# Performance work log

Hardware: AMD Instinct MI355X
Metric: run time of the kernel (lower is better)

The kernel has to match this reference:

```python
import jax, jax.numpy as jnp
import numpy as np

NEG = 1e12


def _sincos(seq_len, dim):
    # SinusoidalPositionEmbedding with merge_mode='zero': [1, S, dim] interleaved (sin, cos)
    pos = jnp.arange(seq_len, dtype=jnp.float32)
    inv = jnp.power(10000.0, -2.0 * jnp.arange(dim // 2, dtype=jnp.float32) / dim)
    emb = pos[:, None] * inv[None, :]                      # [S, dim/2]
    emb = jnp.stack([jnp.sin(emb), jnp.cos(emb)], axis=-1).reshape(seq_len, dim)
    cos_pos = jnp.repeat(emb[:, 1::2], 2, axis=-1)[None]   # [1, S, dim]
    sin_pos = jnp.repeat(emb[:, ::2], 2, axis=-1)[None]    # [1, S, dim]
    return cos_pos, sin_pos


def _rope(x, cos_pos, sin_pos):
    # x: [B, S, d]; rotate pairs: (-x1, x0, -x3, x2, ...)
    x2 = jnp.stack([-x[..., 1::2], x[..., ::2]], axis=-1).reshape(x.shape)
    return x * cos_pos + x2 * sin_pos


def _pointer_head(hidden, mask_f, W1, b1, W2, b2, inner_dim):
    B, S, _ = hidden.shape
    out = hidden @ W1 + b1                                 # [B, S, 2*inner_dim]
    qw, kw = out[..., ::2], out[..., 1::2]                 # [B, S, inner_dim]
    cos_pos, sin_pos = _sincos(S, inner_dim)
    qw = _rope(qw, cos_pos, sin_pos)
    kw = _rope(kw, cos_pos, sin_pos)
    logits = jnp.einsum('bmd,bnd->bmn', qw, kw) / (inner_dim ** 0.5)  # [B, S, S]
    bias = jnp.transpose(hidden @ W2 + b2, (0, 2, 1)) / 2.0           # [B, 2T, S]
    # [B, T, S, S]
    logits = logits[:, None] + bias[:, ::2, None, :] + bias[:, 1::2, :, None]
    # sequence masking on key axis (last) and query axis (second-to-last)
    mk = mask_f[:, None, None, :]
    mq = mask_f[:, None, :, None]
    logits = logits * mq - NEG * (1.0 - mq)
    logits = logits * mk - NEG * (1.0 - mk)
    # strict lower-triangular mask over (m, n)
    tril = jnp.tril(jnp.ones((S, S), dtype=logits.dtype), k=-1)
    logits = logits - tril * NEG
    return logits


def setup_inputs() -> dict:
    key = jax.random.key(0)
    ks = jax.random.split(key, 10)
    B, S, H = 8, 512, 768
    inner_dim, ent_t, arg_t = 64, 12, 16
    s = 0.02
    return {
        'last_hidden_state': jax.random.normal(ks[0], (B, S, H), jnp.float32),
        'attention_mask': jnp.ones((B, S), jnp.int32),
        'W1': jax.random.normal(ks[1], (H, inner_dim * 2), jnp.float32) * s,
        'b1': jax.random.normal(ks[2], (inner_dim * 2,), jnp.float32) * s,
        'W2': jax.random.normal(ks[3], (H, ent_t * 2), jnp.float32) * s,
        'b2': jax.random.normal(ks[4], (ent_t * 2,), jnp.float32) * s,
        'Wa1': jax.random.normal(ks[5], (H, inner_dim * 2), jnp.float32) * s,
        'ba1': jax.random.normal(ks[6], (inner_dim * 2,), jnp.float32) * s,
        'Wa2': jax.random.normal(ks[7], (H, arg_t * 2), jnp.float32) * s,
        'ba2': jax.random.normal(ks[8], (arg_t * 2,), jnp.float32) * s,
    }


def reference(last_hidden_state, attention_mask, W1, b1, W2, b2, Wa1, ba1, Wa2, ba2):
    inner_dim = W1.shape[1] // 2
    mask_f = attention_mask.astype(last_hidden_state.dtype)
    logits = _pointer_head(last_hidden_state, mask_f, W1, b1, W2, b2, inner_dim)
    argument_logits = _pointer_head(last_hidden_state, mask_f, Wa1, ba1, Wa2, ba2, inner_dim)
    return logits, argument_logits
```

## Files before the change

### kernel.cpp

```cpp
#include <hip/hip_runtime.h>
#include <hip/hip_bf16.h>

typedef __attribute__((ext_vector_type(8))) short s16x8;
typedef __attribute__((ext_vector_type(4))) float f32x4;

#define NEGC 1000000000000.0f

constexpr int B_ = 8, S_ = 512, H_ = 768;
constexpr int ENT = 12, ARG = 16;
constexpr int NC = 320;
constexpr int ROWS = B_ * S_;
constexpr size_t OUT_ENT = (size_t)B_ * ENT * S_ * S_;

static __device__ __forceinline__ unsigned short f2bf(float x) {
  return __builtin_bit_cast(unsigned short, __float2bfloat16(x));
}

__global__ __launch_bounds__(256) void k_prep(
    const float* __restrict__ X,
    const float* __restrict__ W1, const float* __restrict__ b1,
    const float* __restrict__ W2, const float* __restrict__ b2,
    const float* __restrict__ Wa1, const float* __restrict__ ba1,
    const float* __restrict__ Wa2, const float* __restrict__ ba2,
    __hip_bfloat16* __restrict__ Xb,
    __hip_bfloat16* __restrict__ Wt,
    float* __restrict__ bcat) {
  int idx = blockIdx.x * 256 + threadIdx.x;
  const int nx = ROWS * H_ / 4;
  if (idx < nx) {
    float4 v = reinterpret_cast<const float4*>(X)[idx];
    ushort4 o;
    o.x = f2bf(v.x); o.y = f2bf(v.y); o.z = f2bf(v.z); o.w = f2bf(v.w);
    reinterpret_cast<ushort4*>(Xb)[idx] = o;
    return;
  }
  idx -= nx;
  if (idx < NC * H_) {
    int n = idx / H_;
    int k = idx - n * H_;
    float v = 0.0f;
    if (n < 128)      v = W1[k * 128 + n];
    else if (n < 152) v = W2[k * 24 + (n - 128)];
    else if (n < 280) v = Wa1[k * 128 + (n - 152)];
    else if (n < 312) v = Wa2[k * 32 + (n - 280)];
    reinterpret_cast<unsigned short*>(Wt)[(size_t)n * H_ + k] = f2bf(v);
    return;
  }
  idx -= NC * H_;
  if (idx < NC) {
    int n = idx;
    float v = 0.0f;
    if (n < 128)      v = b1[n];
    else if (n < 152) v = b2[n - 128];
    else if (n < 280) v = ba1[n - 152];
    else if (n < 312) v = ba2[n - 280];
    bcat[n] = v;
  }
}

__global__ __launch_bounds__(256) void k_gemm(
    const __hip_bfloat16* __restrict__ Xb,
    const __hip_bfloat16* __restrict__ Wt,
    const float* __restrict__ bcat,
    __hip_bfloat16* __restrict__ qwe, __hip_bfloat16* __restrict__ kwe,
    __hip_bfloat16* __restrict__ qwa, __hip_bfloat16* __restrict__ kwa,
    float* __restrict__ kbe, float* __restrict__ qbe,
    float* __restrict__ kba, float* __restrict__ qba) {
  const int lane = threadIdx.x & 63;
  const int wid  = threadIdx.x >> 6;
  const int row0 = blockIdx.y * 64 + (wid >> 1) * 32;
  const int col0 = blockIdx.x * 64 + (wid & 1) * 32;
  const int rl   = lane & 15;
  const int rg   = lane >> 4;
  const int kseg = rg * 8;
  const short* Ws = reinterpret_cast<const short*>(Wt);
  const short* Xs = reinterpret_cast<const short*>(Xb);
  f32x4 acc[2][2] = {};
#pragma unroll 4
  for (int kk = 0; kk < H_; kk += 32) {
    s16x8 a[2], bb[2];
#pragma unroll
    for (int ni = 0; ni < 2; ++ni)
      a[ni] = *reinterpret_cast<const s16x8*>(Ws + (size_t)(col0 + ni * 16 + rl) * H_ + kk + kseg);
#pragma unroll
    for (int mj = 0; mj < 2; ++mj)
      bb[mj] = *reinterpret_cast<const s16x8*>(Xs + (size_t)(row0 + mj * 16 + rl) * H_ + kk + kseg);
#pragma unroll
    for (int ni = 0; ni < 2; ++ni)
#pragma unroll
      for (int mj = 0; mj < 2; ++mj)
        acc[ni][mj] = __builtin_amdgcn_mfma_f32_16x16x32_bf16(a[ni], bb[mj], acc[ni][mj], 0, 0, 0);
  }
#pragma unroll
  for (int ni = 0; ni < 2; ++ni) {
    const int nq = col0 + ni * 16 + rg * 4;
    if (nq >= 312) continue;
    float4 bc = *reinterpret_cast<const float4*>(bcat + nq);
#pragma unroll
    for (int mj = 0; mj < 2; ++mj) {
      const int r = row0 + mj * 16 + rl;
      const int b = r >> 9, mm = r & 511;
      float v0 = acc[ni][mj][0] + bc.x;
      float v1 = acc[ni][mj][1] + bc.y;
      float v2 = acc[ni][mj][2] + bc.z;
      float v3 = acc[ni][mj][3] + bc.w;
      if (nq < 128 || (nq >= 152 && nq < 280)) {
        const bool ent = nq < 128;
        const int p = (ent ? nq : nq - 152) >> 2;
        float inv = exp2f(-(float)p * 0.4152410118609203f);
        float s, c;
        sincosf((float)mm * inv, &s, &c);
        unsigned int qpk = (unsigned int)f2bf(v0 * c - v2 * s) |
                           ((unsigned int)f2bf(v2 * c + v0 * s) << 16);
        unsigned int kpk = (unsigned int)f2bf(v1 * c - v3 * s) |
                           ((unsigned int)f2bf(v3 * c + v1 * s) << 16);
        short* qd = reinterpret_cast<short*>(ent ? qwe : qwa);
        short* kd = reinterpret_cast<short*>(ent ? kwe : kwa);
        *reinterpret_cast<unsigned int*>(qd + (size_t)r * 64 + 2 * p) = qpk;
        *reinterpret_cast<unsigned int*>(kd + (size_t)r * 64 + 2 * p) = kpk;
      } else {
        const bool ent = nq < 152;
        const int base = ent ? 128 : 280;
        const int T = ent ? ENT : ARG;
        float* qb = ent ? qbe : qba;
        float* kb = ent ? kbe : kba;
        float vv[4] = {v0, v1, v2, v3};
#pragma unroll
        for (int q = 0; q < 4; ++q) {
          int e = nq - base + q;
          int t = e >> 1;
          float* dst = (e & 1) ? qb : kb;
          dst[((size_t)b * T + t) * S_ + mm] = vv[q] * 0.5f;
        }
      }
    }
  }
}

__global__ __launch_bounds__(256) void k_bcast(
    const __hip_bfloat16* __restrict__ qwe, const __hip_bfloat16* __restrict__ kwe,
    const __hip_bfloat16* __restrict__ qwa, const __hip_bfloat16* __restrict__ kwa,
    const float* __restrict__ kbe, const float* __restrict__ qbe,
    const float* __restrict__ kba, const float* __restrict__ qba,
    const int* __restrict__ mask,
    float* __restrict__ out) {
  const int lane = threadIdx.x & 63;
  const int w = threadIdx.x >> 6;
  const int b = blockIdx.z;
  const int m0 = blockIdx.y * 64 + w * 16;
  const int n0 = blockIdx.x * 64;
  const int col = lane & 15;
  const int rg = lane >> 4;
  const int kseg = rg * 8;

  int mrow[4];
  float mqv[4], sqv[4];
#pragma unroll
  for (int j = 0; j < 4; ++j) {
    mrow[j] = m0 + rg * 4 + j;
    float mf = (float)mask[b * S_ + mrow[j]];
    mqv[j] = mf; sqv[j] = NEGC * (1.0f - mf);
  }
  int ncol[4];
  float mkv[4], skv[4];
#pragma unroll
  for (int f = 0; f < 4; ++f) {
    ncol[f] = n0 + 16 * f + col;
    float mf = (float)mask[b * S_ + ncol[f]];
    mkv[f] = mf; skv[f] = NEGC * (1.0f - mf);
  }
  float M[4][4], O[4][4];
#pragma unroll
  for (int f = 0; f < 4; ++f)
#pragma unroll
    for (int j = 0; j < 4; ++j) {
      M[f][j] = mqv[j] * mkv[f];
      O[f][j] = sqv[j] * mkv[f] + skv[f] + ((ncol[f] < mrow[j]) ? NEGC : 0.0f);
    }

  auto head = [&](const __hip_bfloat16* qw, const __hip_bfloat16* kw,
                  const float* qb, const float* kb, int T, size_t obase0) {
    const short* qs = reinterpret_cast<const short*>(qw);
    const short* ks = reinterpret_cast<const short*>(kw);
    f32x4 acc[4] = {};
#pragma unroll
    for (int kk = 0; kk < 64; kk += 32) {
      s16x8 a = *reinterpret_cast<const s16x8*>(
          qs + (size_t)(b * S_ + m0 + col) * 64 + kk + kseg);
#pragma unroll
      for (int f = 0; f < 4; ++f) {
        s16x8 bb = *reinterpret_cast<const s16x8*>(
            ks + (size_t)(b * S_ + n0 + 16 * f + col) * 64 + kk + kseg);
        acc[f] = __builtin_amdgcn_mfma_f32_16x16x32_bf16(a, bb, acc[f], 0, 0, 0);
      }
    }
    float accMO[4][4];
#pragma unroll
    for (int f = 0; f < 4; ++f)
#pragma unroll
      for (int j = 0; j < 4; ++j)
        accMO[f][j] = acc[f][j] * 0.125f * M[f][j] - O[f][j];

    for (int t = 0; t < T; ++t) {
      const float* qbp = qb + ((size_t)b * T + t) * S_;
      const float* kbp = kb + ((size_t)b * T + t) * S_;
      float qv[4];
#pragma unroll
      for (int j = 0; j < 4; ++j) qv[j] = qbp[mrow[j]];
      size_t obase = obase0 + (size_t)t * S_ * S_;
#pragma unroll
      for (int f = 0; f < 4; ++f) {
        float kv = kbp[ncol[f]];
#pragma unroll
        for (int j = 0; j < 4; ++j) {
          float v = fmaf(kv + qv[j], M[f][j], accMO[f][j]);
          out[obase + (size_t)mrow[j] * S_ + ncol[f]] = v;
        }
      }
    }
  };

  head(qwe, kwe, qbe, kbe, ENT, (size_t)b * ENT * S_ * S_);
  head(qwa, kwa, qba, kba, ARG, OUT_ENT + (size_t)b * ARG * S_ * S_);
}

extern "C" void kernel_launch(void* const* d_in, const int* in_sizes, int n_in,
                              void* d_out, int out_size, void* d_ws, size_t ws_size,
                              hipStream_t stream) {
  (void)in_sizes; (void)n_in; (void)out_size; (void)ws_size;
  const float* X   = (const float*)d_in[0];
  const int* mask  = (const int*)d_in[1];
  const float* W1  = (const float*)d_in[2];
  const float* b1  = (const float*)d_in[3];
  const float* W2  = (const float*)d_in[4];
  const float* b2  = (const float*)d_in[5];
  const float* Wa1 = (const float*)d_in[6];
  const float* ba1 = (const float*)d_in[7];
  const float* Wa2 = (const float*)d_in[8];
  const float* ba2 = (const float*)d_in[9];
  float* out = (float*)d_out;

  char* ws = (char*)d_ws;
  size_t off = 0;
  auto walloc = [&](size_t bytes) -> void* {
    void* p = ws + off;
    off += (bytes + 255) & ~(size_t)255;
    return p;
  };
  __hip_bfloat16* Xb  = (__hip_bfloat16*)walloc((size_t)ROWS * H_ * 2);
  __hip_bfloat16* Wt  = (__hip_bfloat16*)walloc((size_t)NC * H_ * 2);
  float* bcat         = (float*)walloc((size_t)NC * 4);
  __hip_bfloat16* qwe = (__hip_bfloat16*)walloc((size_t)ROWS * 64 * 2);
  __hip_bfloat16* kwe = (__hip_bfloat16*)walloc((size_t)ROWS * 64 * 2);
  __hip_bfloat16* qwa = (__hip_bfloat16*)walloc((size_t)ROWS * 64 * 2);
  __hip_bfloat16* kwa = (__hip_bfloat16*)walloc((size_t)ROWS * 64 * 2);
  float* kbe = (float*)walloc((size_t)B_ * ENT * S_ * 4);
  float* qbe = (float*)walloc((size_t)B_ * ENT * S_ * 4);
  float* kba = (float*)walloc((size_t)B_ * ARG * S_ * 4);
  float* qba = (float*)walloc((size_t)B_ * ARG * S_ * 4);

  const int prep_tasks = ROWS * H_ / 4 + NC * H_ + NC;
  k_prep<<<dim3((prep_tasks + 255) / 256), dim3(256), 0, stream>>>(
      X, W1, b1, W2, b2, Wa1, ba1, Wa2, ba2, Xb, Wt, bcat);
  k_gemm<<<dim3(NC / 64, ROWS / 64), dim3(256), 0, stream>>>(
      Xb, Wt, bcat, qwe, kwe, qwa, kwa, kbe, qbe, kba, qba);
  k_bcast<<<dim3(8, 8, 8), dim3(256), 0, stream>>>(
      qwe, kwe, qwa, kwa, kbe, qbe, kba, qba, mask, out);
}
```

Before: 75.16 us.

## Restructure broadcast kernel to stage QK tile in LDS and emit vectorized row stores

Result: slower. 81.10 us (+7.9%).

```diff
diff --git a/kernel.cpp b/kernel.cpp
--- a/kernel.cpp
+++ b/kernel.cpp
@@ -14,6 +14,9 @@
 
 static __device__ __forceinline__ unsigned short f2bf(float x) {
   return __builtin_bit_cast(unsigned short, __float2bfloat16(x));
+}
+static __device__ __forceinline__ float bf2f(unsigned short u) {
+  return __builtin_bit_cast(float, (unsigned int)u << 16);
 }
 
 __global__ __launch_bounds__(256) void k_prep(
@@ -144,84 +147,108 @@
     const float* __restrict__ kba, const float* __restrict__ qba,
     const int* __restrict__ mask,
     float* __restrict__ out) {
-  const int lane = threadIdx.x & 63;
-  const int w = threadIdx.x >> 6;
-  const int b = blockIdx.z;
-  const int m0 = blockIdx.y * 64 + w * 16;
-  const int n0 = blockIdx.x * 64;
-  const int col = lane & 15;
-  const int rg = lane >> 4;
-  const int kseg = rg * 8;
-
-  int mrow[4];
-  float mqv[4], sqv[4];
-#pragma unroll
-  for (int j = 0; j < 4; ++j) {
-    mrow[j] = m0 + rg * 4 + j;
-    float mf = (float)mask[b * S_ + mrow[j]];
-    mqv[j] = mf; sqv[j] = NEGC * (1.0f - mf);
-  }
-  int ncol[4];
-  float mkv[4], skv[4];
-#pragma unroll
-  for (int f = 0; f < 4; ++f) {
-    ncol[f] = n0 + 16 * f + col;
-    float mf = (float)mask[b * S_ + ncol[f]];
-    mkv[f] = mf; skv[f] = NEGC * (1.0f - mf);
-  }
-  float M[4][4], O[4][4];
-#pragma unroll
-  for (int f = 0; f < 4; ++f)
-#pragma unroll
-    for (int j = 0; j < 4; ++j) {
-      M[f][j] = mqv[j] * mkv[f];
-      O[f][j] = sqv[j] * mkv[f] + skv[f] + ((ncol[f] < mrow[j]) ? NEGC : 0.0f);
-    }
-
-  auto head = [&](const __hip_bfloat16* qw, const __hip_bfloat16* kw,
-                  const float* qb, const float* kb, int T, size_t obase0) {
-    const short* qs = reinterpret_cast<const short*>(qw);
-    const short* ks = reinterpret_cast<const short*>(kw);
-    f32x4 acc[4] = {};
-#pragma unroll
-    for (int kk = 0; kk < 64; kk += 32) {
-      s16x8 a = *reinterpret_cast<const s16x8*>(
-          qs + (size_t)(b * S_ + m0 + col) * 64 + kk + kseg);
-#pragma unroll
-      for (int f = 0; f < 4; ++f) {
-        s16x8 bb = *reinterpret_cast<const s16x8*>(
-            ks + (size_t)(b * S_ + n0 + 16 * f + col) * 64 + kk + kseg);
-        acc[f] = __builtin_amdgcn_mfma_f32_16x16x32_bf16(a, bb, acc[f], 0, 0, 0);
-      }
-    }
-    float accMO[4][4];
-#pragma unroll
-    for (int f = 0; f < 4; ++f)
-#pragma unroll
-      for (int j = 0; j < 4; ++j)
-        accMO[f][j] = acc[f][j] * 0.125f * M[f][j] - O[f][j];
-
-    for (int t = 0; t < T; ++t) {
-      const float* qbp = qb + ((size_t)b * T + t) * S_;
-      const float* kbp = kb + ((size_t)b * T + t) * S_;
-      float qv[4];
-#pragma unroll
-      for (int j = 0; j < 4; ++j) qv[j] = qbp[mrow[j]];
-      size_t obase = obase0 + (size_t)t * S_ * S_;
-#pragma unroll
-      for (int f = 0; f < 4; ++f) {
-        float kv = kbp[ncol[f]];
-#pragma unroll
-        for (int j = 0; j < 4; ++j) {
-          float v = fmaf(kv + qv[j], M[f][j], accMO[f][j]);
-          out[obase + (size_t)mrow[j] * S_ + ncol[f]] = v;
-        }
-      }
-    }
-  };
-
-  head(qwe, kwe, qbe, kbe, ENT, (size_t)b * ENT * S_ * S_);
-  head(qwa, kwa, qba, kba, ARG, OUT_ENT + (size_t)b * ARG * S_ * S_);
+  __shared__ unsigned short qk_lds[32][520];
+  const int tid  = threadIdx.x;
+  const int lane = tid & 63;
+  const int w    = tid >> 6;
+  const int b    = blockIdx.z;
+  const int m0   = blockIdx.y * 32;
+  const int c    = blockIdx.x;
+  const bool ent = c < 3;
+  const int t0   = (ent ? c : c - 3) * 4;
+  const int T    = ent ? ENT : ARG;
+  const short* qs = reinterpret_cast<const short*>(ent ? qwe : qwa);
+  const short* ks = reinterpret_cast<const short*>(ent ? kwe : kwa);
+  const float* qb = ent ? qbe : qba;
+  const float* kb = ent ? kbe : kba;
+  const size_t obase0 = ent ? (size_t)b * ENT * S_ * S_
+                            : OUT_ENT + (size_t)b * ARG * S_ * S_;
+
+  {
+    const int cl = lane & 15, rg = lane >> 4, kseg = rg * 8;
+    const int mf = w & 1, nh = w >> 1;
+    const size_t qrow = (size_t)(b * S_ + m0 + mf * 16 + cl) * 64;
+    s16x8 bq0 = *reinterpret_cast<const s16x8*>(qs + qrow + kseg);
+    s16x8 bq1 = *reinterpret_cast<const s16x8*>(qs + qrow + 32 + kseg);
+#pragma unroll
+    for (int g = 0; g < 2; ++g) {
+      f32x4 acc[8];
+#pragma unroll
+      for (int f = 0; f < 8; ++f) {
+        const int n = nh * 256 + (g * 8 + f) * 16;
+        const size_t krow = (size_t)(b * S_ + n + cl) * 64;
+        s16x8 ak0 = *reinterpret_cast<const s16x8*>(ks + krow + kseg);
+        s16x8 ak1 = *reinterpret_cast<const s16x8*>(ks + krow + 32 + kseg);
+        f32x4 z = {};
+        acc[f] = __builtin_amdgcn_mfma_f32_16x16x32_bf16(ak0, bq0, z, 0, 0, 0);
+        acc[f] = __builtin_amdgcn_mfma_f32_16x16x32_bf16(ak1, bq1, acc[f], 0, 0, 0);
+      }
+#pragma unroll
+      for (int f = 0; f < 8; ++f) {
+        const int n = nh * 256 + (g * 8 + f) * 16 + rg * 4;
+        ushort4 o;
+        o.x = f2bf(acc[f][0] * 0.125f);
+        o.y = f2bf(acc[f][1] * 0.125f);
+        o.z = f2bf(acc[f][2] * 0.125f);
+        o.w = f2bf(acc[f][3] * 0.125f);
+        *reinterpret_cast<ushort4*>(&qk_lds[mf * 16 + cl][n]) = o;
+      }
+    }
+  }
+  __syncthreads();
+
+  const int nA = lane * 4;
+  const int nB = 256 + lane * 4;
+  const int* mp = mask + b * S_;
+  float mkA[4], mkB[4], skA[4], skB[4];
+#pragma unroll
+  for (int i = 0; i < 4; ++i) {
+    mkA[i] = (float)mp[nA + i];
+    skA[i] = NEGC * (1.0f - mkA[i]);
+    mkB[i] = (float)mp[nB + i];
+    skB[i] = NEGC * (1.0f - mkB[i]);
+  }
+  float kvA[4][4], kvB[4][4];
+#pragma unroll
+  for (int t = 0; t < 4; ++t) {
+    const float* kbp = kb + ((size_t)b * T + t0 + t) * S_;
+    f32x4 a = *reinterpret_cast<const f32x4*>(kbp + nA);
+    f32x4 bb = *reinterpret_cast<const f32x4*>(kbp + nB);
+#pragma unroll
+    for (int i = 0; i < 4; ++i) { kvA[t][i] = a[i]; kvB[t][i] = bb[i]; }
+  }
+
+  for (int rr = 0; rr < 8; ++rr) {
+    const int r = w * 8 + rr;
+    const int rglob = m0 + r;
+    const float mq = (float)mp[rglob];
+    const float sq = NEGC * (1.0f - mq);
+    ushort4 ua = *reinterpret_cast<const ushort4*>(&qk_lds[r][nA]);
+    ushort4 ub = *reinterpret_cast<const ushort4*>(&qk_lds[r][nB]);
+    float qkA[4] = {bf2f(ua.x), bf2f(ua.y), bf2f(ua.z), bf2f(ua.w)};
+    float qkB[4] = {bf2f(ub.x), bf2f(ub.y), bf2f(ub.z), bf2f(ub.w)};
+    float MA[4], nOA[4], MB[4], nOB[4];
+#pragma unroll
+    for (int i = 0; i < 4; ++i) {
+      MA[i]  = mq * mkA[i];
+      nOA[i] = -(sq * mkA[i] + skA[i] + ((nA + i < rglob) ? NEGC : 0.0f));
+      MB[i]  = mq * mkB[i];
+      nOB[i] = -(sq * mkB[i] + skB[i] + ((nB + i < rglob) ? NEGC : 0.0f));
+    }
+#pragma unroll
+    for (int t = 0; t < 4; ++t) {
+      const float qv = qb[((size_t)b * T + t0 + t) * S_ + rglob];
+      f32x4 vA, vB;
+#pragma unroll
+      for (int i = 0; i < 4; ++i) {
+        vA[i] = fmaf(qkA[i] + (kvA[t][i] + qv), MA[i], nOA[i]);
+        vB[i] = fmaf(qkB[i] + (kvB[t][i] + qv), MB[i], nOB[i]);
+      }
+      float* op = out + obase0 + (size_t)(t0 + t) * S_ * S_ + (size_t)rglob * S_;
+      *reinterpret_cast<f32x4*>(op + nA) = vA;
+      *reinterpret_cast<f32x4*>(op + nB) = vB;
+    }
+  }
 }
 
 extern "C" void kernel_launch(void* const* d_in, const int* in_sizes, int n_in,
@@ -264,6 +291,6 @@
       X, W1, b1, W2, b2, Wa1, ba1, Wa2, ba2, Xb, Wt, bcat);
   k_gemm<<<dim3(NC / 64, ROWS / 64), dim3(256), 0, stream>>>(
       Xb, Wt, bcat, qwe, kwe, qwa, kwa, kbe, qbe, kba, qba);
-  k_bcast<<<dim3(8, 8, 8), dim3(256), 0, stream>>>(
+  k_bcast<<<dim3(7, 16, 8), dim3(256), 0, stream>>>(
       qwe, kwe, qwa, kwa, kbe, qbe, kba, qba, mask, out);
 }
```
